# Kernel tuning notes

Measured on AMD Instinct MI355X. Metric: run time of the kernel, lower is better.

Reference implementation:

```python
import jax, jax.numpy as jnp
import numpy as np

N_NODES = 4096
N_EDGES = 32768
IN_FEAT = 256
OUT_FEAT = 128
HID = 64
IN_HEAD = 64
OUT_HEAD = 5
NEG_SLOPE = 0.2
EPS = 1e-16


def setup_inputs() -> dict:
    key = jax.random.key(0)
    ks = jax.random.split(key, 12)
    x = jax.random.normal(ks[0], (N_NODES, IN_FEAT), dtype=jnp.float32)
    src = jax.random.randint(ks[1], (N_EDGES,), 0, N_NODES)
    dst = jax.random.randint(ks[2], (N_EDGES,), 0, N_NODES)
    edge_index = jnp.stack([src, dst]).astype(jnp.int64)
    s1 = 1.0 / np.sqrt(IN_FEAT)
    s2 = 1.0 / np.sqrt(HID * IN_HEAD)
    W1 = jax.random.normal(ks[3], (IN_FEAT, IN_HEAD * HID), dtype=jnp.float32) * s1
    att_src1 = jax.random.normal(ks[4], (IN_HEAD, HID), dtype=jnp.float32) * 0.1
    att_dst1 = jax.random.normal(ks[5], (IN_HEAD, HID), dtype=jnp.float32) * 0.1
    b1 = jnp.zeros((IN_HEAD * HID,), dtype=jnp.float32)
    W2 = jax.random.normal(ks[6], (IN_HEAD * HID, OUT_HEAD * OUT_FEAT), dtype=jnp.float32) * s2
    att_src2 = jax.random.normal(ks[7], (OUT_HEAD, OUT_FEAT), dtype=jnp.float32) * 0.1
    att_dst2 = jax.random.normal(ks[8], (OUT_HEAD, OUT_FEAT), dtype=jnp.float32) * 0.1
    b2 = jnp.zeros((OUT_FEAT,), dtype=jnp.float32)
    return {"x": x, "edge_index": edge_index, "W1": W1, "att_src1": att_src1,
            "att_dst1": att_dst1, "b1": b1, "W2": W2, "att_src2": att_src2,
            "att_dst2": att_dst2, "b2": b2}


def _gat_conv(x, W, att_src, att_dst, bias, src, dst, heads, out_c, concat):
    # x: [N, F_in]; returns [N, heads*out_c] (concat) or [N, out_c] (mean)
    n = x.shape[0]
    h = (x @ W).reshape(n, heads, out_c)                       # [N,H,C]
    a_src = jnp.sum(h * att_src, axis=-1)                      # [N,H]
    a_dst = jnp.sum(h * att_dst, axis=-1)                      # [N,H]
    e = jax.nn.leaky_relu(a_src[src] + a_dst[dst], NEG_SLOPE)  # [E,H]
    # segment softmax over edges grouped by destination node (PyG softmax)
    m = jax.ops.segment_max(e, dst, num_segments=n)            # [N,H]
    ex = jnp.exp(e - m[dst])
    denom = jax.ops.segment_sum(ex, dst, num_segments=n)       # [N,H]
    alpha = ex / (denom[dst] + EPS)                            # [E,H]
    out = jax.ops.segment_sum(alpha[:, :, None] * h[src], dst, num_segments=n)  # [N,H,C]
    out = out.reshape(n, heads * out_c) if concat else out.mean(axis=1)
    return out + bias


def reference(x, edge_index, W1, att_src1, att_dst1, b1, W2, att_src2, att_dst2, b2):
    n = x.shape[0]
    # PyG GATConv default: add self loops
    loop = jnp.arange(n, dtype=edge_index.dtype)
    src = jnp.concatenate([edge_index[0], loop])
    dst = jnp.concatenate([edge_index[1], loop])
    # dropout layers are identity in eval mode
    h = _gat_conv(x, W1, att_src1, att_dst1, b1, src, dst, IN_HEAD, HID, True)
    h = jax.nn.elu(h)
    h = _gat_conv(h, W2, att_src2, att_dst2, b2, src, dst, OUT_HEAD, OUT_FEAT, False)
    s = jnp.mean(h, axis=0)
    return jnp.tanh(s)
```

## Files before the change

### kernel.cpp

```cpp
#include <hip/hip_runtime.h>
#include <hip/hip_bf16.h>

#define N_NODES 4096
#define NE      32768
#define E_TOT   (NE + N_NODES)
#define IN_FEAT 256
#define HID     64
#define IN_HEAD 64
#define F1      4096
#define OUT_HEAD 5
#define OUT_FEAT 128
#define F2      640
#define NEG_SLOPE 0.2f
#define EPS_A   1e-16f

typedef __bf16 bf16;
typedef bf16 bf16x8 __attribute__((ext_vector_type(8)));
typedef bf16 bf16x4 __attribute__((ext_vector_type(4)));
typedef float f32x4 __attribute__((ext_vector_type(4)));

__device__ inline void async_cp16(bf16* lds, const bf16* g) {
    __builtin_amdgcn_global_load_lds(
        (const __attribute__((address_space(1))) unsigned int*)g,
        (__attribute__((address_space(3))) unsigned int*)lds, 16, 0, 0);
}

__global__ void hist_kernel(const int* __restrict__ edst, int* counts) {
    int e = blockIdx.x * 256 + threadIdx.x;
    if (e >= E_TOT) return;
    int d = (e < NE) ? edst[e] : (e - NE);
    atomicAdd(&counts[d], 1);
}

__global__ void scan_kernel(const int* __restrict__ counts,
                            int* __restrict__ row_start, int* __restrict__ cursor) {
    __shared__ int part[256];
    __shared__ int pre[257];
    int t = threadIdx.x;
    int base = t * 16;
    int local[16];
    int s = 0;
#pragma unroll
    for (int i = 0; i < 16; ++i) { local[i] = s; s += counts[base + i]; }
    part[t] = s;
    __syncthreads();
    if (t == 0) {
        int r = 0;
        for (int i = 0; i < 256; ++i) { pre[i] = r; r += part[i]; }
        pre[256] = r;
    }
    __syncthreads();
    int off = pre[t];
#pragma unroll
    for (int i = 0; i < 16; ++i) {
        int v = off + local[i];
        row_start[base + i] = v;
        cursor[base + i] = v;
    }
    if (t == 0) row_start[N_NODES] = pre[256];
}

__global__ void scatter_kernel(const int* __restrict__ esrc,
                               const int* __restrict__ edst,
                               int* cursor, int* __restrict__ srclist) {
    int e = blockIdx.x * 256 + threadIdx.x;
    if (e >= E_TOT) return;
    int d = (e < NE) ? edst[e] : (e - NE);
    int s = (e < NE) ? esrc[e] : (e - NE);
    int slot = atomicAdd(&cursor[d], 1);
    srclist[slot] = s;
}

#define PB_X   512
#define PB_W1  1024
#define PB_W2  2560
__global__ __launch_bounds__(256)
void prep_kernel(const float* __restrict__ x, bf16* __restrict__ xb,
                 const float* __restrict__ W1, bf16* __restrict__ W1T,
                 const float* __restrict__ W2, bf16* __restrict__ W2T,
                 const float* __restrict__ as1, const float* __restrict__ ad1,
                 bf16* __restrict__ w1s, bf16* __restrict__ w1d) {
    __shared__ float tile[32][33];
    int b = blockIdx.x, t = threadIdx.x;
    if (b < PB_X) {
        int i = b * 256 + t;
        f32x4 a = *(const f32x4*)(x + (size_t)i * 8);
        f32x4 c = *(const f32x4*)(x + (size_t)i * 8 + 4);
        bf16x8 r;
        r[0] = (bf16)a[0]; r[1] = (bf16)a[1]; r[2] = (bf16)a[2]; r[3] = (bf16)a[3];
        r[4] = (bf16)c[0]; r[5] = (bf16)c[1]; r[6] = (bf16)c[2]; r[7] = (bf16)c[3];
        *(bf16x8*)(xb + (size_t)i * 8) = r;
    } else if (b < PB_X + PB_W1 + PB_W2) {
        const float* S; bf16* D; int R, C, gx, gy;
        if (b < PB_X + PB_W1) {
            int bb = b - PB_X;
            S = W1; D = W1T; R = IN_FEAT; C = F1;
            gx = bb % (F1 / 32); gy = bb / (F1 / 32);
        } else {
            int bb = b - PB_X - PB_W1;
            S = W2; D = W2T; R = F1; C = F2;
            gx = bb % (F2 / 32); gy = bb / (F2 / 32);
        }
        int tx = t & 31, ty = t >> 5;
        int c0 = gx * 32, r0 = gy * 32;
#pragma unroll
        for (int i = 0; i < 4; ++i)
            tile[ty + i * 8][tx] = S[(size_t)(r0 + ty + i * 8) * C + c0 + tx];
        __syncthreads();
#pragma unroll
        for (int i = 0; i < 4; ++i)
            D[(size_t)(c0 + ty + i * 8) * R + r0 + tx] = (bf16)tile[tx][ty + i * 8];
    } else {
        int id = (b - PB_X - PB_W1 - PB_W2) * 256 + t;
        int k = id >> 6, h = id & 63;
        const float* wrow = W1 + (size_t)k * F1 + h * HID;
        const float* a1 = as1 + h * HID;
        const float* a2 = ad1 + h * HID;
        float s = 0.f, d = 0.f;
#pragma unroll 8
        for (int c = 0; c < HID; ++c) {
            float w = wrow[c];
            s += w * a1[c];
            d += w * a2[c];
        }
        w1s[id] = (bf16)s;
        w1d[id] = (bf16)d;
    }
}

template <int SPLITK, bool SWZ, typename TC>
__global__ __launch_bounds__(256)
void gemm128_kernel(const bf16* __restrict__ A, const bf16* __restrict__ BT,
                    TC* __restrict__ C, int M, int N, int K) {
    __shared__ bf16 As[128][64];
    __shared__ bf16 Bs[128][64];
    const int tid  = threadIdx.x;
    const int wave = tid >> 6, lane = tid & 63;
    const int quad = lane >> 4, lr = lane & 15;
    int nb, mb, zb;
    if constexpr (SWZ) {
        int bid = blockIdx.x;
        zb = bid & 7;
        int q = bid >> 3;
        int gp = q / 5;
        nb = q - gp * 5;
        mb = gp;
    } else {
        nb = blockIdx.x; mb = blockIdx.y; zb = blockIdx.z;
    }
    const int m0 = mb * 128, n0 = nb * 128;
    const int kchunk = K / SPLITK;
    const int kbeg = zb * kchunk;
    const int wm = (wave >> 1) * 64;
    const int wn = (wave & 1) * 64;
    TC* Cz = C + (size_t)zb * M * N;

    const int srow = lane >> 3;
    const int scol = ((lane & 7) ^ srow) * 8;
    const int xk = lr & 7;

    f32x4 acc[4][4] = {};

    for (int kk = 0; kk < kchunk; kk += 64) {
        int k0 = kbeg + kk;
#pragma unroll
        for (int c = 0; c < 4; ++c) {
            int r = wave * 32 + c * 8;
            async_cp16(&As[r][0], A + (size_t)(m0 + r + srow) * K + k0 + scol);
            async_cp16(&Bs[r][0], BT + (size_t)(n0 + r + srow) * K + k0 + scol);
        }
        __syncthreads();

#pragma unroll
        for (int ks = 0; ks < 2; ++ks) {
            int ch = ((ks * 4 + quad) ^ xk) * 8;
            bf16x8 af[4], bfr[4];
#pragma unroll
            for (int mt = 0; mt < 4; ++mt)
                af[mt] = *(const bf16x8*)(&As[wm + mt * 16 + lr][ch]);
#pragma unroll
            for (int nt = 0; nt < 4; ++nt)
                bfr[nt] = *(const bf16x8*)(&Bs[wn + nt * 16 + lr][ch]);
#pragma unroll
            for (int mt = 0; mt < 4; ++mt)
#pragma unroll
                for (int nt = 0; nt < 4; ++nt)
                    acc[mt][nt] = __builtin_amdgcn_mfma_f32_16x16x32_bf16(
                        af[mt], bfr[nt], acc[mt][nt], 0, 0, 0);
        }
        __syncthreads();
    }

#pragma unroll
    for (int mt = 0; mt < 4; ++mt)
#pragma unroll
        for (int nt = 0; nt < 4; ++nt) {
            int row0 = m0 + wm + mt * 16 + quad * 4;
            int col = n0 + wn + nt * 16 + lr;
#pragma unroll
            for (int r = 0; r < 4; ++r)
                Cz[(size_t)(row0 + r) * N + col] = (TC)acc[mt][nt][r];
        }
}

__global__ __launch_bounds__(256)
void gemv1_kernel(const float* __restrict__ x,
                  const bf16* __restrict__ w1s, const bf16* __restrict__ w1d,
                  float* __restrict__ a_src, float* __restrict__ a_dst) {
    int wave = threadIdx.x >> 6, lane = threadIdx.x & 63;
    int n = blockIdx.x * 4 + wave;
    const float* xr = x + (size_t)n * IN_FEAT;
    float s = 0.f, d = 0.f;
    for (int k0 = 0; k0 < IN_FEAT; k0 += 4) {
        f32x4 xv = *(const f32x4*)(xr + k0);
#pragma unroll
        for (int j = 0; j < 4; ++j) {
            float xs = xv[j];
            s += xs * (float)w1s[(k0 + j) * IN_HEAD + lane];
            d += xs * (float)w1d[(k0 + j) * IN_HEAD + lane];
        }
    }
    a_src[n * IN_HEAD + lane] = s;
    a_dst[n * IN_HEAD + lane] = d;
}

__global__ __launch_bounds__(64)
void agg1_kernel(const int* __restrict__ row_start,
                 const int* __restrict__ srclist,
                 const float* __restrict__ a_src, const float* __restrict__ a_dst,
                 const bf16* __restrict__ H1, const float* __restrict__ b1,
                 bf16* __restrict__ h_elu) {
    int bid = blockIdx.x;
    int c = bid & 7;
    int d = bid >> 3;
    int lane = threadIdx.x;
    int gh = c * 8 + (lane >> 3);
    int beg = row_start[d], deg = row_start[d + 1] - beg;
    float adst = a_dst[d * IN_HEAD + gh];
    int fbase = c * 512 + lane * 8;
    const float* asg = a_src + gh;

    auto SL = [&](int i) { return srclist[beg + (i < deg ? i : deg - 1)]; };

    int s0 = SL(0), s1 = SL(1), s2 = SL(2), s3 = SL(3);
    float la0 = asg[(size_t)s0 * IN_HEAD];
    bf16x8 v0 = *(const bf16x8*)(H1 + (size_t)s0 * F1 + fbase);
    float la1 = asg[(size_t)s1 * IN_HEAD];
    bf16x8 v1 = *(const bf16x8*)(H1 + (size_t)s1 * F1 + fbase);
    float la2 = asg[(size_t)s2 * IN_HEAD];
    bf16x8 v2 = *(const bf16x8*)(H1 + (size_t)s2 * F1 + fbase);
    float la3 = asg[(size_t)s3 * IN_HEAD];
    bf16x8 v3 = *(const bf16x8*)(H1 + (size_t)s3 * F1 + fbase);
    int s4 = SL(4), s5 = SL(5);

    float m = -1e30f, den = 0.f;
    float acc[8] = {};
    for (int i = 0; i < deg; ++i) {
        int sn = SL(i + 6);
        float la4 = asg[(size_t)s4 * IN_HEAD];
        bf16x8 v4 = *(const bf16x8*)(H1 + (size_t)s4 * F1 + fbase);

        float l = la0 + adst;
        l = l > 0.f ? l : NEG_SLOPE * l;
        if (l > m + 12.f) {
            float r = __expf(m - l);
            den *= r;
#pragma unroll
            for (int k = 0; k < 8; ++k) acc[k] *= r;
            m = l;
        }
        float w = __expf(l - m);
        den += w;
#pragma unroll
        for (int k = 0; k < 8; ++k) acc[k] += w * (float)v0[k];

        la0 = la1; v0 = v1;
        la1 = la2; v1 = v2;
        la2 = la3; v2 = v3;
        la3 = la4; v3 = v4;
        s4 = s5; s5 = sn;
    }
    float dinv = 1.f / (den + EPS_A);

    bf16x8 o;
#pragma unroll
    for (int j = 0; j < 8; ++j) {
        float v = acc[j] * dinv + b1[fbase + j];
        o[j] = (bf16)(v > 0.f ? v : (__expf(v) - 1.f));
    }
    *(bf16x8*)(h_elu + (size_t)d * F1 + fbase) = o;
}

__global__ __launch_bounds__(192)
void fold2_kernel(const bf16* __restrict__ Hp,
                  const float* __restrict__ as2, const float* __restrict__ ad2,
                  float* __restrict__ H2,
                  float* __restrict__ a_src, float* __restrict__ a_dst) {
    int n = blockIdx.x, t = threadIdx.x;
    if (t >= 160) return;
    int h = t >> 5;
    f32x4 sum = {};
#pragma unroll
    for (int z = 0; z < 8; ++z) {
        bf16x4 v = *(const bf16x4*)(Hp + (size_t)z * N_NODES * F2 + (size_t)n * F2 + t * 4);
        sum[0] += (float)v[0]; sum[1] += (float)v[1];
        sum[2] += (float)v[2]; sum[3] += (float)v[3];
    }
    *(f32x4*)(H2 + (size_t)n * F2 + t * 4) = sum;
    f32x4 ws = *(const f32x4*)(as2 + t * 4);
    f32x4 wd = *(const f32x4*)(ad2 + t * 4);
    float s = sum[0] * ws[0] + sum[1] * ws[1] + sum[2] * ws[2] + sum[3] * ws[3];
    float d = sum[0] * wd[0] + sum[1] * wd[1] + sum[2] * wd[2] + sum[3] * wd[3];
#pragma unroll
    for (int o = 1; o <= 16; o <<= 1) {
        s += __shfl_xor(s, o);
        d += __shfl_xor(d, o);
    }
    if ((t & 31) == 0) {
        a_src[n * OUT_HEAD + h] = s;
        a_dst[n * OUT_HEAD + h] = d;
    }
}

__global__ void stats2_kernel(const int* __restrict__ row_start,
                              const int* __restrict__ srclist,
                              const float* __restrict__ a_src,
                              const float* __restrict__ a_dst,
                              float* __restrict__ m2, float* __restrict__ dinv2,
                              float* __restrict__ beta) {
    int id = blockIdx.x * 256 + threadIdx.x;
    if (id >= N_NODES * OUT_HEAD) return;
    beta[id] = 0.f;
    int d = id / OUT_HEAD, h = id - d * OUT_HEAD;
    int beg = row_start[d], deg = row_start[d + 1] - beg;
    float adst = a_dst[id];
    auto SL = [&](int i) { return srclist[beg + (i < deg ? i : deg - 1)]; };
    int s0 = SL(0), s1 = SL(1);
    float la0 = a_src[s0 * OUT_HEAD + h];
    float m = -1e30f, den = 0.f;
    for (int i = 0; i < deg; ++i) {
        int s2 = SL(i + 2);
        float la1 = a_src[s1 * OUT_HEAD + h];
        float l = la0 + adst;
        l = l > 0.f ? l : NEG_SLOPE * l;
        if (l > m + 12.f) { den *= __expf(m - l); m = l; }
        den += __expf(l - m);
        la0 = la1; s1 = s2;
    }
    m2[id] = m;
    dinv2[id] = 1.f / (den + EPS_A);
}

__global__ void beta_kernel(const int* __restrict__ es, const int* __restrict__ ed,
                            const float* __restrict__ a_src, const float* __restrict__ a_dst,
                            const float* __restrict__ m2, const float* __restrict__ dinv2,
                            float* __restrict__ beta,
                            float* __restrict__ acc_out, int* __restrict__ ticket) {
    int id = blockIdx.x * 256 + threadIdx.x;
    if (id < 8 * OUT_FEAT) acc_out[id] = 0.f;
    else if (id == 8 * OUT_FEAT) *ticket = 0;
    if (id >= E_TOT * OUT_HEAD) return;
    int e = id / OUT_HEAD, h = id - e * OUT_HEAD;
    int s = (e < NE) ? es[e] : (e - NE);
    int d = (e < NE) ? ed[e] : (e - NE);
    float l = a_src[s * OUT_HEAD + h] + a_dst[d * OUT_HEAD + h];
    l = l > 0.f ? l : NEG_SLOPE * l;
    float alpha = __expf(l - m2[d * OUT_HEAD + h]) * dinv2[d * OUT_HEAD + h];
    atomicAdd(&beta[s * OUT_HEAD + h], alpha);
}

__global__ __launch_bounds__(256)
void wsum_kernel(const float* __restrict__ H2, const float* __restrict__ beta,
                 float* __restrict__ acc_out, const float* __restrict__ b2,
                 float* __restrict__ out, int* __restrict__ ticket) {
    __shared__ float buf[F2];
    __shared__ int lastblk;
    int t = threadIdx.x;
    int n0 = blockIdx.x * 32;
    int h = t >> 5;
    float a0 = 0.f, a1 = 0.f, a2 = 0.f, a3 = 0.f;
    if (t < 160) {
        for (int i = 0; i < 32; ++i) {
            int s = n0 + i;
            float bh = beta[s * OUT_HEAD + h];
            f32x4 v = *(const f32x4*)(H2 + (size_t)s * F2 + t * 4);
            a0 += bh * v[0]; a1 += bh * v[1];
            a2 += bh * v[2]; a3 += bh * v[3];
        }
        buf[t * 4 + 0] = a0; buf[t * 4 + 1] = a1;
        buf[t * 4 + 2] = a2; buf[t * 4 + 3] = a3;
    }
    __syncthreads();
    if (t < OUT_FEAT) {
        float s = 0.f;
#pragma unroll
        for (int hh = 0; hh < OUT_HEAD; ++hh) s += buf[hh * OUT_FEAT + t];
        atomicAdd(&acc_out[(blockIdx.x & 7) * OUT_FEAT + t], s);
    }
    __syncthreads();
    if (t == 0) {
        __threadfence();
        lastblk = (atomicAdd(ticket, 1) == (int)gridDim.x - 1);
    }
    __syncthreads();
    if (lastblk && t < OUT_FEAT) {
        float tot = 0.f;
#pragma unroll
        for (int k = 0; k < 8; ++k)
            tot += atomicAdd(&acc_out[k * OUT_FEAT + t], 0.0f);
        out[t] = tanhf(tot * (1.f / (OUT_HEAD * (float)N_NODES)) + b2[t]);
    }
}

extern "C" void kernel_launch(void* const* d_in, const int* in_sizes, int n_in,
                              void* d_out, int out_size, void* d_ws, size_t ws_size,
                              hipStream_t stream) {
    const float* x        = (const float*)d_in[0];
    const int*   ei       = (const int*)d_in[1];
    const float* W1       = (const float*)d_in[2];
    const float* att_src1 = (const float*)d_in[3];
    const float* att_dst1 = (const float*)d_in[4];
    const float* b1       = (const float*)d_in[5];
    const float* W2       = (const float*)d_in[6];
    const float* att_src2 = (const float*)d_in[7];
    const float* att_dst2 = (const float*)d_in[8];
    const float* b2       = (const float*)d_in[9];
    float* out = (float*)d_out;

    const int* esrc = ei;
    const int* edst = ei + NE;

    char* p = (char*)d_ws;
    auto bump = [&](size_t bytes) {
        void* r = (void*)p;
        p += (bytes + 255) & ~(size_t)255;
        return r;
    };
    bf16*  H1     = (bf16*)bump((size_t)N_NODES * F1 * 2);
    bf16*  h_elu  = (bf16*)bump((size_t)N_NODES * F1 * 2);
    bf16*  Hp     = (bf16*)bump((size_t)8 * N_NODES * F2 * 2);
    float* H2     = (float*)bump((size_t)N_NODES * F2 * 4);
    bf16*  xb     = (bf16*)bump((size_t)N_NODES * IN_FEAT * 2);
    bf16*  W1T    = (bf16*)bump((size_t)F1 * IN_FEAT * 2);
    bf16*  W2T    = (bf16*)bump((size_t)F2 * F1 * 2);
    bf16*  w1s    = (bf16*)bump((size_t)IN_FEAT * IN_HEAD * 2);
    bf16*  w1d    = (bf16*)bump((size_t)IN_FEAT * IN_HEAD * 2);
    float* a_src1 = (float*)bump((size_t)N_NODES * IN_HEAD * 4);
    float* a_dst1 = (float*)bump((size_t)N_NODES * IN_HEAD * 4);
    float* a_src2 = (float*)bump((size_t)N_NODES * OUT_HEAD * 4);
    float* a_dst2 = (float*)bump((size_t)N_NODES * OUT_HEAD * 4);
    float* m2     = (float*)bump((size_t)N_NODES * OUT_HEAD * 4);
    float* dinv2  = (float*)bump((size_t)N_NODES * OUT_HEAD * 4);
    int*   row_start = (int*)bump((N_NODES + 1) * 4);
    int*   cursor  = (int*)bump(N_NODES * 4);
    int*   srclist = (int*)bump(E_TOT * 4);
    int*   counts  = (int*)bump(N_NODES * 4);
    float* beta    = (float*)bump((size_t)N_NODES * OUT_HEAD * 4);
    float* acc_out = (float*)bump((size_t)8 * OUT_FEAT * 4);
    int*   ticket  = (int*)bump(4);

    hipMemsetAsync(counts, 0, N_NODES * 4, stream);
    hist_kernel<<<(E_TOT + 255) / 256, 256, 0, stream>>>(edst, counts);
    scan_kernel<<<1, 256, 0, stream>>>(counts, row_start, cursor);
    scatter_kernel<<<(E_TOT + 255) / 256, 256, 0, stream>>>(
        esrc, edst, cursor, srclist);

    prep_kernel<<<PB_X + PB_W1 + PB_W2 + 64, 256, 0, stream>>>(
        x, xb, W1, W1T, W2, W2T, att_src1, att_dst1, w1s, w1d);

    gemm128_kernel<1, false, bf16>
        <<<dim3(F1 / 128, N_NODES / 128, 1), 256, 0, stream>>>(
        xb, W1T, H1, N_NODES, F1, IN_FEAT);
    gemv1_kernel<<<N_NODES / 4, 256, 0, stream>>>(x, w1s, w1d, a_src1, a_dst1);
    agg1_kernel<<<N_NODES * 8, 64, 0, stream>>>(
        row_start, srclist, a_src1, a_dst1, H1, b1, h_elu);

    gemm128_kernel<8, true, bf16><<<1280, 256, 0, stream>>>(
        h_elu, W2T, Hp, N_NODES, F2, F1);
    fold2_kernel<<<N_NODES, 192, 0, stream>>>(
        Hp, att_src2, att_dst2, H2, a_src2, a_dst2);
    stats2_kernel<<<(N_NODES * OUT_HEAD + 255) / 256, 256, 0, stream>>>(
        row_start, srclist, a_src2, a_dst2, m2, dinv2, beta);
    beta_kernel<<<(E_TOT * OUT_HEAD + 255) / 256, 256, 0, stream>>>(
        esrc, edst, a_src2, a_dst2, m2, dinv2, beta, acc_out, ticket);
    wsum_kernel<<<N_NODES / 32, 256, 0, stream>>>(
        H2, beta, acc_out, b2, out, ticket);
}
```

Baseline: 244.5 us.

## Fuse histogram into prep, merge layer-1 GEMM with GEMV, halve GEMM2 split-K

The edge histogram now runs as extra blocks of the prep kernel, and the layer-1 GEMM and the attention GEMV share one launch, which removes several kernel launches and their serialization gaps. The second GEMM changes from split-K 8 to split-K 4 with a remapped block swizzle. This halves the partial-sum buffer written to and read back by fold2. In exchange, each GEMM2 block has a longer K loop, and there are half as many blocks to fill the GPU.

```diff
diff --git a/kernel.cpp b/kernel.cpp
--- a/kernel.cpp
+++ b/kernel.cpp
@@ -25,13 +25,6 @@
         (__attribute__((address_space(3))) unsigned int*)lds, 16, 0, 0);
 }
 
-__global__ void hist_kernel(const int* __restrict__ edst, int* counts) {
-    int e = blockIdx.x * 256 + threadIdx.x;
-    if (e >= E_TOT) return;
-    int d = (e < NE) ? edst[e] : (e - NE);
-    atomicAdd(&counts[d], 1);
-}
-
 __global__ void scan_kernel(const int* __restrict__ counts,
                             int* __restrict__ row_start, int* __restrict__ cursor) {
     __shared__ int part[256];
@@ -74,12 +67,16 @@
 #define PB_X   512
 #define PB_W1  1024
 #define PB_W2  2560
+#define PB_ATT 64
+#define PB_TOT (PB_X + PB_W1 + PB_W2 + PB_ATT)
+#define PB_HIST 144
 __global__ __launch_bounds__(256)
 void prep_kernel(const float* __restrict__ x, bf16* __restrict__ xb,
                  const float* __restrict__ W1, bf16* __restrict__ W1T,
                  const float* __restrict__ W2, bf16* __restrict__ W2T,
                  const float* __restrict__ as1, const float* __restrict__ ad1,
-                 bf16* __restrict__ w1s, bf16* __restrict__ w1d) {
+                 bf16* __restrict__ w1s, bf16* __restrict__ w1d,
+                 const int* __restrict__ edst, int* __restrict__ counts) {
     __shared__ float tile[32][33];
     int b = blockIdx.x, t = threadIdx.x;
     if (b < PB_X) {
@@ -110,7 +107,7 @@
 #pragma unroll
         for (int i = 0; i < 4; ++i)
             D[(size_t)(c0 + ty + i * 8) * R + r0 + tx] = (bf16)tile[tx][ty + i * 8];
-    } else {
+    } else if (b < PB_TOT) {
         int id = (b - PB_X - PB_W1 - PB_W2) * 256 + t;
         int k = id >> 6, h = id & 63;
         const float* wrow = W1 + (size_t)k * F1 + h * HID;
@@ -125,29 +122,25 @@
         }
         w1s[id] = (bf16)s;
         w1d[id] = (bf16)d;
-    }
-}
-
-template <int SPLITK, bool SWZ, typename TC>
-__global__ __launch_bounds__(256)
-void gemm128_kernel(const bf16* __restrict__ A, const bf16* __restrict__ BT,
-                    TC* __restrict__ C, int M, int N, int K) {
+    } else {
+        int e = (b - PB_TOT) * 256 + t;
+        if (e < E_TOT) {
+            int d = (e < NE) ? edst[e] : (e - NE);
+            atomicAdd(&counts[d], 1);
+        }
+    }
+}
+
+template <int SPLITK, typename TC>
+__device__ __forceinline__
+void gemm_body(const bf16* __restrict__ A, const bf16* __restrict__ BT,
+               TC* __restrict__ C, int M, int N, int K,
+               int nb, int mb, int zb) {
     __shared__ bf16 As[128][64];
     __shared__ bf16 Bs[128][64];
     const int tid  = threadIdx.x;
     const int wave = tid >> 6, lane = tid & 63;
     const int quad = lane >> 4, lr = lane & 15;
-    int nb, mb, zb;
-    if constexpr (SWZ) {
-        int bid = blockIdx.x;
-        zb = bid & 7;
-        int q = bid >> 3;
-        int gp = q / 5;
-        nb = q - gp * 5;
-        mb = gp;
-    } else {
-        nb = blockIdx.x; mb = blockIdx.y; zb = blockIdx.z;
-    }
     const int m0 = mb * 128, n0 = nb * 128;
     const int kchunk = K / SPLITK;
     const int kbeg = zb * kchunk;
@@ -204,24 +197,43 @@
 }
 
 __global__ __launch_bounds__(256)
-void gemv1_kernel(const float* __restrict__ x,
-                  const bf16* __restrict__ w1s, const bf16* __restrict__ w1d,
-                  float* __restrict__ a_src, float* __restrict__ a_dst) {
-    int wave = threadIdx.x >> 6, lane = threadIdx.x & 63;
-    int n = blockIdx.x * 4 + wave;
-    const float* xr = x + (size_t)n * IN_FEAT;
-    float s = 0.f, d = 0.f;
-    for (int k0 = 0; k0 < IN_FEAT; k0 += 4) {
-        f32x4 xv = *(const f32x4*)(xr + k0);
-#pragma unroll
-        for (int j = 0; j < 4; ++j) {
-            float xs = xv[j];
-            s += xs * (float)w1s[(k0 + j) * IN_HEAD + lane];
-            d += xs * (float)w1d[(k0 + j) * IN_HEAD + lane];
-        }
-    }
-    a_src[n * IN_HEAD + lane] = s;
-    a_dst[n * IN_HEAD + lane] = d;
+void gemm2_kernel(const bf16* __restrict__ A, const bf16* __restrict__ BT,
+                  bf16* __restrict__ C) {
+    int bid = blockIdx.x;
+    int xx = bid & 7, q = bid >> 3;
+    int gp = q / 5; int nb = q - gp * 5;
+    int g = gp * 8 + xx;
+    int mb = g >> 2, zb = g & 3;
+    gemm_body<4, bf16>(A, BT, C, N_NODES, F2, F1, nb, mb, zb);
+}
+
+__global__ __launch_bounds__(256)
+void layer1_kernel(const bf16* __restrict__ xb, const bf16* __restrict__ W1T,
+                   bf16* __restrict__ H1,
+                   const float* __restrict__ x,
+                   const bf16* __restrict__ w1s, const bf16* __restrict__ w1d,
+                   float* __restrict__ a_src, float* __restrict__ a_dst) {
+    int bid = blockIdx.x;
+    if (bid < 1024) {
+        gemm_body<1, bf16>(xb, W1T, H1, N_NODES, F1, IN_FEAT,
+                           bid & 31, bid >> 5, 0);
+    } else {
+        int wave = threadIdx.x >> 6, lane = threadIdx.x & 63;
+        int n = (bid - 1024) * 4 + wave;
+        const float* xr = x + (size_t)n * IN_FEAT;
+        float s = 0.f, d = 0.f;
+        for (int k0 = 0; k0 < IN_FEAT; k0 += 4) {
+            f32x4 xv = *(const f32x4*)(xr + k0);
+#pragma unroll
+            for (int j = 0; j < 4; ++j) {
+                float xs = xv[j];
+                s += xs * (float)w1s[(k0 + j) * IN_HEAD + lane];
+                d += xs * (float)w1d[(k0 + j) * IN_HEAD + lane];
+            }
+        }
+        a_src[n * IN_HEAD + lane] = s;
+        a_dst[n * IN_HEAD + lane] = d;
+    }
 }
 
 __global__ __launch_bounds__(64)
@@ -301,7 +313,7 @@
     int h = t >> 5;
     f32x4 sum = {};
 #pragma unroll
-    for (int z = 0; z < 8; ++z) {
+    for (int z = 0; z < 4; ++z) {
         bf16x4 v = *(const bf16x4*)(Hp + (size_t)z * N_NODES * F2 + (size_t)n * F2 + t * 4);
         sum[0] += (float)v[0]; sum[1] += (float)v[1];
         sum[2] += (float)v[2]; sum[3] += (float)v[3];
@@ -438,7 +450,7 @@
     };
     bf16*  H1     = (bf16*)bump((size_t)N_NODES * F1 * 2);
     bf16*  h_elu  = (bf16*)bump((size_t)N_NODES * F1 * 2);
-    bf16*  Hp     = (bf16*)bump((size_t)8 * N_NODES * F2 * 2);
+    bf16*  Hp     = (bf16*)bump((size_t)4 * N_NODES * F2 * 2);
     float* H2     = (float*)bump((size_t)N_NODES * F2 * 4);
     bf16*  xb     = (bf16*)bump((size_t)N_NODES * IN_FEAT * 2);
     bf16*  W1T    = (bf16*)bump((size_t)F1 * IN_FEAT * 2);
@@ -460,23 +472,18 @@
     int*   ticket  = (int*)bump(4);
 
     hipMemsetAsync(counts, 0, N_NODES * 4, stream);
-    hist_kernel<<<(E_TOT + 255) / 256, 256, 0, stream>>>(edst, counts);
+    prep_kernel<<<PB_TOT + PB_HIST, 256, 0, stream>>>(
+        x, xb, W1, W1T, W2, W2T, att_src1, att_dst1, w1s, w1d, edst, counts);
     scan_kernel<<<1, 256, 0, stream>>>(counts, row_start, cursor);
     scatter_kernel<<<(E_TOT + 255) / 256, 256, 0, stream>>>(
         esrc, edst, cursor, srclist);
 
-    prep_kernel<<<PB_X + PB_W1 + PB_W2 + 64, 256, 0, stream>>>(
-        x, xb, W1, W1T, W2, W2T, att_src1, att_dst1, w1s, w1d);
-
-    gemm128_kernel<1, false, bf16>
-        <<<dim3(F1 / 128, N_NODES / 128, 1), 256, 0, stream>>>(
-        xb, W1T, H1, N_NODES, F1, IN_FEAT);
-    gemv1_kernel<<<N_NODES / 4, 256, 0, stream>>>(x, w1s, w1d, a_src1, a_dst1);
+    layer1_kernel<<<2048, 256, 0, stream>>>(
+        xb, W1T, H1, x, w1s, w1d, a_src1, a_dst1);
     agg1_kernel<<<N_NODES * 8, 64, 0, stream>>>(
         row_start, srclist, a_src1, a_dst1, H1, b1, h_elu);
 
-    gemm128_kernel<8, true, bf16><<<1280, 256, 0, stream>>>(
-        h_elu, W2T, Hp, N_NODES, F2, F1);
+    gemm2_kernel<<<640, 256, 0, stream>>>(h_elu, W2T, Hp);
     fold2_kernel<<<N_NODES, 192, 0, stream>>>(
         Hp, att_src2, att_dst2, H2, a_src2, a_dst2);
     stats2_kernel<<<(N_NODES * OUT_HEAD + 255) / 256, 256, 0, stream>>>(
```

After: 238.7 us. 1.02x faster.
